# Kernel optimization log

Measured on AMD Instinct MI355X. Metric: run time of the kernel, lower is better.

Reference implementation:

```python
import jax, jax.numpy as jnp
import numpy as np

B, C, T, W, H = 4, 128, 16, 64, 64


def setup_inputs() -> dict:
    key = jax.random.key(0)
    ks = jax.random.split(key, 5)
    Cq = C // 8
    return {
        "x": jax.random.normal(ks[0], (B, C, T, W, H), jnp.float32),
        # stacked params for the 3 cells (T, W, H order, as in nn.Sequential)
        "Wq": jax.random.normal(ks[1], (3, Cq, C), jnp.float32) * 0.05,
        "bq": jnp.zeros((3, Cq), jnp.float32),
        "Wk": jax.random.normal(ks[2], (3, Cq, C), jnp.float32) * 0.05,
        "bk": jnp.zeros((3, Cq), jnp.float32),
        "Wv": jax.random.normal(ks[3], (3, C, C), jnp.float32) * 0.05,
        "bv": jnp.zeros((3, C), jnp.float32),
        # gamma is init to 0 in torch (identity); small random so the test is nontrivial
        "gamma": jax.random.normal(ks[4], (3,), jnp.float32) * 0.1,
    }


def _conv1x1(x, w, b):
    # 1x1x1 Conv3d == channel contraction
    return jnp.einsum('bcthw,oc->bothw', x, w) + b[None, :, None, None, None]


def _cell(x, wq, bq, wk, bk, wv, bv, gamma, attn_dim):
    # Faithful to torch: raw contiguous .view() == row-major reshape.
    Bb, Cc, Tt, Ww, Hh = x.shape
    q = _conv1x1(x, wq, bq).reshape(Bb, attn_dim, -1)   # (B, A, N)
    k = _conv1x1(x, wk, bk).reshape(Bb, -1, attn_dim)   # (B, N, A)  (pooling_factor=1 -> MaxPool identity)
    attn = jax.nn.softmax(jnp.matmul(q, k), axis=-1)    # (B, A, A)
    v = _conv1x1(x, wv, bv).reshape(Bb, -1, attn_dim)   # (B, M, A), M = C*T*W*H/A
    out = jnp.matmul(v, attn.swapaxes(1, 2))            # (B, M, A)
    out = out.reshape(Bb, Cc, Ww, Hh, Tt).transpose(0, 1, 4, 2, 3)  # -> (B, C, T, W, H)
    return gamma * out + x


def reference(x, Wq, bq, Wk, bk, Wv, bv, gamma):
    _, _, Tt, Ww, Hh = x.shape
    attn_dims = (Tt, Ww, Hh)  # cells with attn_id 'T', 'W', 'H'
    for i in range(3):
        x = _cell(x, Wq[i], bq[i], Wk[i], bk[i], Wv[i], bv[i], gamma[i], attn_dims[i])
    return x
```

## Files before the change

kernel.cpp:

```cpp
#include <hip/hip_runtime.h>

#define BB 4
#define CC 128
#define CQ 16
#define TDIM 16
#define SS 65536
#define CS (CC*SS)
#define NBLK 256

typedef unsigned short u16;
typedef unsigned int   u32;

typedef __bf16 bf16x8v __attribute__((ext_vector_type(8)));
typedef float  floatx4v __attribute__((ext_vector_type(4)));

__device__ __forceinline__ u16 f2bf(float f) {
    u32 u = __float_as_uint(f);
    u32 r = (u + 0x7fffu + ((u >> 16) & 1u)) >> 16;
    return (u16)r;
}
__device__ __forceinline__ void unpack8(uint4 r, float* f) {
    f[0] = __uint_as_float(r.x << 16); f[1] = __uint_as_float(r.x & 0xffff0000u);
    f[2] = __uint_as_float(r.y << 16); f[3] = __uint_as_float(r.y & 0xffff0000u);
    f[4] = __uint_as_float(r.z << 16); f[5] = __uint_as_float(r.z & 0xffff0000u);
    f[6] = __uint_as_float(r.w << 16); f[7] = __uint_as_float(r.w & 0xffff0000u);
}
__device__ __forceinline__ bf16x8v ld_bf8(const void* p) {
    union { uint4 u; bf16x8v b; } x;
    x.u = *(const uint4*)p;
    return x.b;
}

__global__ __launch_bounds__(256) void wconv_kernel(
    const float* __restrict__ Wq, const float* __restrict__ Wk, const float* __restrict__ Wv,
    const float* __restrict__ bq, const float* __restrict__ bk, const float* __restrict__ bv,
    u16* __restrict__ wbf, float* __restrict__ bias)
{
    const int idx = blockIdx.x * 256 + threadIdx.x;
    const int cell = idx / 20480;
    const int j = idx - cell * 20480;
    const int o = j >> 7, c = j & 127;
    float v;
    if (o < 16)      v = Wq[(cell * 16 + o) * 128 + c];
    else if (o < 32) v = Wk[(cell * 16 + (o - 16)) * 128 + c];
    else             v = Wv[(cell * 128 + (o - 32)) * 128 + c];
    wbf[idx] = f2bf(v);
    if (idx < 480) {
        const int cl = idx / 160, oo = idx - cl * 160;
        float b = (oo < 16) ? bq[cl * 16 + oo]
                : (oo < 32) ? bk[cl * 16 + oo - 16]
                :             bv[cl * 128 + oo - 32];
        bias[idx] = b;
    }
}

__global__ __launch_bounds__(256, 2) void qkv_mfma_kernel(
    const float* __restrict__ x,
    const u16* __restrict__ wbf, const float* __restrict__ bias,
    float* __restrict__ qf, float* __restrict__ kf, u16* __restrict__ vf)
{
    __shared__ u16 xT[128 * 128];
    const int t  = threadIdx.x;
    const int b  = blockIdx.y;
    const int s0 = blockIdx.x << 7;
    const float* xb = x + (size_t)b * CS;

    {
        const int sl = t & 127;
        const int cb = (t >> 7) << 3;
        const float* xs = xb + s0 + sl;
        const u32 rowb = (u32)sl << 8;
        const u32 swz  = (u32)(sl & 7) << 4;
#pragma unroll 2
        for (int p = 0; p < 8; p++) {
            const int c0 = p * 16 + cb;
            float f[8];
#pragma unroll
            for (int j = 0; j < 8; j++) f[j] = xs[(size_t)(c0 + j) * SS];
            uint4 pk;
            pk.x = (u32)f2bf(f[0]) | ((u32)f2bf(f[1]) << 16);
            pk.y = (u32)f2bf(f[2]) | ((u32)f2bf(f[3]) << 16);
            pk.z = (u32)f2bf(f[4]) | ((u32)f2bf(f[5]) << 16);
            pk.w = (u32)f2bf(f[6]) | ((u32)f2bf(f[7]) << 16);
            *(uint4*)((char*)xT + ((rowb + (u32)(c0 << 1)) ^ swz)) = pk;
        }
    }
    __syncthreads();

    const int lane = t & 63;
    const int wv   = t >> 6;
    const int mh   = wv >> 1;
    const int sh   = wv & 1;
    const int ln15 = lane & 15;
    const int lhi  = lane >> 4;

    floatx4v acc[5][4] = {};

    const u16* abase = wbf + ((mh * 80 + ln15) << 7) + (lhi << 3);
    const u32 swzB = (u32)(ln15 & 7) << 4;
    const int sbase = sh * 64 + ln15;

#pragma unroll
    for (int ks = 0; ks < 4; ks++) {
        bf16x8v af[5];
#pragma unroll
        for (int mi = 0; mi < 5; mi++)
            af[mi] = ld_bf8(abase + (mi << 11) + (ks << 5));
#pragma unroll
        for (int nt = 0; nt < 4; nt++) {
            const u32 off = (((u32)(sbase + nt * 16) << 8)
                           + (u32)((ks << 6) + (lhi << 4))) ^ swzB;
            bf16x8v bf = ld_bf8((const char*)xT + off);
#pragma unroll
            for (int mi = 0; mi < 5; mi++)
                acc[mi][nt] = __builtin_amdgcn_mfma_f32_16x16x32_bf16(
                                  af[mi], bf, acc[mi][nt], 0, 0, 0);
        }
    }

    float* qb = qf + (size_t)b * ((size_t)CQ * SS);
    float* kb = kf + (size_t)b * ((size_t)CQ * SS);
    u16*   vb = vf + (size_t)b * (size_t)CS;

#pragma unroll
    for (int mi = 0; mi < 5; mi++) {
        const int o0 = mh * 80 + mi * 16 + lhi * 4;
        float bia[4];
        *(float4*)bia = *(const float4*)(bias + o0);
#pragma unroll
        for (int nt = 0; nt < 4; nt++) {
            const int s = s0 + sh * 64 + nt * 16 + ln15;
            if (o0 < 16) {
#pragma unroll
                for (int r = 0; r < 4; r++)
                    qb[(size_t)(o0 + r) * SS + s] = acc[mi][nt][r] + bia[r];
            } else if (o0 < 32) {
#pragma unroll
                for (int r = 0; r < 4; r++)
                    kb[(size_t)(o0 - 16 + r) * SS + s] = acc[mi][nt][r] + bia[r];
            } else {
#pragma unroll
                for (int r = 0; r < 4; r++)
                    vb[(size_t)(o0 - 32 + r) * SS + s] = f2bf(acc[mi][nt][r] + bia[r]);
            }
        }
    }
}

template <int A>
__global__ __launch_bounds__(256) void logits_part_kernel(
    const float* __restrict__ qf, const float* __restrict__ kf,
    float* __restrict__ part)
{
    constexpr int N = (CQ * SS) / A;
    constexpr int NCHUNK = N / NBLK;
    constexpr int NLOG = (NCHUNK == 64) ? 6 : 8;
    __shared__ float qs[A][NCHUNK + 1];
    __shared__ float ks[NCHUNK][A];
    const int t  = threadIdx.x;
    const int b  = blockIdx.y;
    const int n0 = blockIdx.x << NLOG;
    const float* qb = qf + (size_t)b * ((size_t)CQ * SS);
    const float* kb = kf + (size_t)b * ((size_t)CQ * SS);

    for (int idx = t; idx < A * NCHUNK; idx += 256) {
        int a1 = idx >> NLOG, n = idx & (NCHUNK - 1);
        qs[a1][n] = qb[(size_t)a1 * N + n0 + n];
    }
    float* ksf = &ks[0][0];
    for (int idx = t; idx < NCHUNK * A; idx += 256)
        ksf[idx] = kb[(size_t)n0 * A + idx];
    __syncthreads();

    float* pb = part + ((size_t)b * NBLK + blockIdx.x) * (A * A);

    if constexpr (A == 16) {
        int a1 = t >> 4, a2 = t & 15;
        float s = 0.f;
#pragma unroll 8
        for (int n = 0; n < NCHUNK; n++) s += qs[a1][n] * ks[n][a2];
        pb[t] = s;
    } else {
        int a1  = t & 63;
        int a2b = (t >> 6) * 16;
        float acc[16];
#pragma unroll
        for (int j = 0; j < 16; j++) acc[j] = 0.f;
        for (int n = 0; n < NCHUNK; n++) {
            float q = qs[a1][n];
#pragma unroll
            for (int j = 0; j < 16; j++) acc[j] += q * ks[n][a2b + j];
        }
        float* dst = pb + t * 16;
        *(float4*)(dst)      = make_float4(acc[0],  acc[1],  acc[2],  acc[3]);
        *(float4*)(dst + 4)  = make_float4(acc[4],  acc[5],  acc[6],  acc[7]);
        *(float4*)(dst + 8)  = make_float4(acc[8],  acc[9],  acc[10], acc[11]);
        *(float4*)(dst + 12) = make_float4(acc[12], acc[13], acc[14], acc[15]);
    }
}

template <int A>
__global__ __launch_bounds__(256) void reduce_softmax_kernel(
    const float* __restrict__ part, float* __restrict__ attn)
{
    constexpr int NG = 256 / A;
    __shared__ float red[NG][A];
    const int a1 = blockIdx.x;
    const int b  = blockIdx.y;
    const int t  = threadIdx.x;
    const int a2 = t & (A - 1);
    const int g  = t >> ((A == 16) ? 4 : 6);
    const float* pb = part + (size_t)b * NBLK * (A * A);

    int off;
    if constexpr (A == 16) off = a1 * 16 + a2;
    else                   off = a1 * 16 + ((a2 >> 4) << 10) + (a2 & 15);

    float s0 = 0.f, s1 = 0.f, s2 = 0.f, s3 = 0.f;
    for (int blk = g; blk < NBLK; blk += 4 * NG) {
        s0 += pb[(size_t)(blk         ) * (A * A) + off];
        s1 += pb[(size_t)(blk +     NG) * (A * A) + off];
        s2 += pb[(size_t)(blk + 2 * NG) * (A * A) + off];
        s3 += pb[(size_t)(blk + 3 * NG) * (A * A) + off];
    }
    red[g][a2] = (s0 + s1) + (s2 + s3);
    __syncthreads();

    if (t < A) {
        float l = 0.f;
#pragma unroll
        for (int gg = 0; gg < NG; gg++) l += red[gg][t];
        float m = l;
#pragma unroll
        for (int o2 = A / 2; o2 > 0; o2 >>= 1) m = fmaxf(m, __shfl_xor(m, o2, 64));
        float e = expf(l - m);
        float s = e;
#pragma unroll
        for (int o2 = A / 2; o2 > 0; o2 >>= 1) s += __shfl_xor(s, o2, 64);
        attn[((size_t)b << 12) + a1 * A + t] = e / s;
    }
}

__global__ __launch_bounds__(256) void out16_kernel(
    const float* __restrict__ x, const u16* __restrict__ vf,
    const float* __restrict__ attn, const float* __restrict__ gptr,
    float* __restrict__ y)
{
    const int b = blockIdx.y;
    const u32 u = blockIdx.x * 256u + threadIdx.x;
    const float g = *gptr;
    const float* ab = attn + ((size_t)b << 12);
    const float* xb = x + (size_t)b * CS;
    float*       yb = y + (size_t)b * CS;
    const u16*   vr = vf + (size_t)b * CS + (size_t)u * 16;

    uint4 r0 = *(const uint4*)(vr);
    uint4 r1 = *(const uint4*)(vr + 8);
    float v0[8], v1[8];
    unpack8(r0, v0); unpack8(r1, v1);

    const size_t base = ((size_t)(u >> 12) << 16) + (u & 4095u);
#pragma unroll
    for (int tt = 0; tt < 16; tt++) {
        const float* ar = ab + tt * 16;
        float4 a0 = *(const float4*)(ar);
        float4 a1 = *(const float4*)(ar + 4);
        float4 a2 = *(const float4*)(ar + 8);
        float4 a3 = *(const float4*)(ar + 12);
        float acc = v0[0]*a0.x + v0[1]*a0.y + v0[2]*a0.z + v0[3]*a0.w
                  + v0[4]*a1.x + v0[5]*a1.y + v0[6]*a1.z + v0[7]*a1.w
                  + v1[0]*a2.x + v1[1]*a2.y + v1[2]*a2.z + v1[3]*a2.w
                  + v1[4]*a3.x + v1[5]*a3.y + v1[6]*a3.z + v1[7]*a3.w;
        const size_t i = base + ((size_t)tt << 12);
        yb[i] = g * acc + xb[i];
    }
}

__device__ __forceinline__ u32 atoff(int r, int c) {
    return (((u32)r << 8) + ((u32)c << 2)) ^ (((u32)(r >> 4) & 3u) << 4);
}

__global__ __launch_bounds__(256) void out64_kernel(
    const float* __restrict__ x, const u16* __restrict__ vf,
    const float* __restrict__ attn, const float* __restrict__ gptr,
    float* __restrict__ y)
{
    __shared__ float atf[4096];
    const int b = blockIdx.y;
    const int t = threadIdx.x;
    const float g = *gptr;
    const float* ab = attn + ((size_t)b << 12);
    {
        char* atb = (char*)atf;
        for (int idx = t; idx < 4096; idx += 256)
            *(float*)(atb + atoff(idx >> 6, idx & 63)) = ab[idx];
    }
    __syncthreads();

    const u32 u   = blockIdx.x * 256u + t;
    const int hlow = u & 3;
    const int h2   = (u >> 2) & 15;
    const int w    = (u >> 6) & 63;
    const int c    = u >> 12;
    const int n    = (c << 10) + (w << 4) + h2;

    const u16*   vr = vf + (size_t)b * CS + (size_t)n * 64;
    const float* xb = x + (size_t)b * CS;
    float*       yb = y + (size_t)b * CS;

    float acc[16];
#pragma unroll
    for (int i = 0; i < 16; i++) acc[i] = 0.f;

    const char* atb = (const char*)atf;
#pragma unroll
    for (int a2b = 0; a2b < 64; a2b += 8) {
        uint4 rv = *(const uint4*)(vr + a2b);
        float v[8];
        unpack8(rv, v);
#pragma unroll
        for (int tt = 0; tt < 16; tt++) {
            const int r = hlow * 16 + tt;
            float4 p0 = *(const float4*)(atb + atoff(r, a2b));
            float4 p1 = *(const float4*)(atb + atoff(r, a2b + 4));
            acc[tt] += v[0]*p0.x + v[1]*p0.y + v[2]*p0.z + v[3]*p0.w
                     + v[4]*p1.x + v[5]*p1.y + v[6]*p1.z + v[7]*p1.w;
        }
    }

    const size_t base = ((size_t)c << 16) + ((u32)w << 6) + (h2 << 2) + hlow;
#pragma unroll
    for (int tt = 0; tt < 16; tt++) {
        const size_t i = base + ((size_t)tt << 12);
        yb[i] = g * acc[tt] + xb[i];
    }
}

extern "C" void kernel_launch(void* const* d_in, const int* in_sizes, int n_in,
                              void* d_out, int out_size, void* d_ws, size_t ws_size,
                              hipStream_t stream)
{
    (void)in_sizes; (void)n_in; (void)out_size;
    const float* x0    = (const float*)d_in[0];
    const float* Wq    = (const float*)d_in[1];
    const float* bq    = (const float*)d_in[2];
    const float* Wk    = (const float*)d_in[3];
    const float* bk    = (const float*)d_in[4];
    const float* Wv    = (const float*)d_in[5];
    const float* bv    = (const float*)d_in[6];
    const float* gamma = (const float*)d_in[7];
    float* y = (float*)d_out;

    const size_t MiB = (size_t)1 << 20;
    const size_t need4 = 4 * (28 * MiB + 16384) + 160 * 128 * 3 * 2 + 3 * 160 * 4;
    const int nb = (ws_size >= need4) ? 4 : 1;

    char* ws = (char*)d_ws;
    float* qf    = (float*)ws;
    float* kf    = (float*)(ws + (size_t)nb * 4  * MiB);
    u16*   vf    = (u16*)  (ws + (size_t)nb * 8  * MiB);
    float* part  = (float*)(ws + (size_t)nb * 24 * MiB);
    float* attnp = (float*)(ws + (size_t)nb * 28 * MiB);
    u16*   wbf3  = (u16*)  (ws + (size_t)nb * 28 * MiB + (size_t)nb * 16384);
    float* bias3 = (float*)(ws + (size_t)nb * 28 * MiB + (size_t)nb * 16384
                               + 160 * 128 * 3 * 2);

    wconv_kernel<<<240, 256, 0, stream>>>(Wq, Wk, Wv, bq, bk, bv, wbf3, bias3);

    for (int cell = 0; cell < 3; cell++) {
        const u16*   wc = wbf3  + (size_t)cell * 160 * 128;
        const float* bc = bias3 + (size_t)cell * 160;
        for (int b0 = 0; b0 < BB; b0 += nb) {
            const float* xin = ((cell == 0) ? x0 : (const float*)y) + (size_t)b0 * CS;
            float* yb = y + (size_t)b0 * CS;

            qkv_mfma_kernel<<<dim3(512, nb), 256, 0, stream>>>(xin, wc, bc, qf, kf, vf);

            if (cell == 0) {
                logits_part_kernel<16><<<dim3(NBLK, nb), 256, 0, stream>>>(qf, kf, part);
                reduce_softmax_kernel<16><<<dim3(16, nb), 256, 0, stream>>>(part, attnp);
                out16_kernel<<<dim3(2048, nb), 256, 0, stream>>>(xin, vf, attnp, gamma + cell, yb);
            } else {
                logits_part_kernel<64><<<dim3(NBLK, nb), 256, 0, stream>>>(qf, kf, part);
                reduce_softmax_kernel<64><<<dim3(64, nb), 256, 0, stream>>>(part, attnp);
                out64_kernel<<<dim3(2048, nb), 256, 0, stream>>>(xin, vf, attnp, gamma + cell, yb);
            }
        }
    }
}
```

Before: 666.3 us.

## Use MFMA for the 64-dim attention output and widen the QKV projection blocks

The output stage of the W and H cells now does the v·attnᵀ product with bf16 MFMA instructions, replacing the scalar FMA loop that read fp32 attention from LDS. The softmax kernel writes an extra bf16 copy of the attention matrix, which is loaded straight into registers, and the output is written as float4 stores. Separately, the QKV projection kernel moves to 512 threads per block, each wave covering a smaller spatial slice with fewer accumulators. This trades cheaper compute and less register pressure for extra bf16 rounding of the attention weights, which may affect accuracy.

```diff
diff --git a/kernel.cpp b/kernel.cpp
--- a/kernel.cpp
+++ b/kernel.cpp
@@ -54,7 +54,7 @@
     }
 }
 
-__global__ __launch_bounds__(256, 2) void qkv_mfma_kernel(
+__global__ __launch_bounds__(512, 4) void qkv_mfma_kernel(
     const float* __restrict__ x,
     const u16* __restrict__ wbf, const float* __restrict__ bias,
     float* __restrict__ qf, float* __restrict__ kf, u16* __restrict__ vf)
@@ -71,9 +71,9 @@
         const float* xs = xb + s0 + sl;
         const u32 rowb = (u32)sl << 8;
         const u32 swz  = (u32)(sl & 7) << 4;
-#pragma unroll 2
-        for (int p = 0; p < 8; p++) {
-            const int c0 = p * 16 + cb;
+#pragma unroll
+        for (int p = 0; p < 4; p++) {
+            const int c0 = p * 32 + cb;
             float f[8];
 #pragma unroll
             for (int j = 0; j < 8; j++) f[j] = xs[(size_t)(c0 + j) * SS];
@@ -89,16 +89,16 @@
 
     const int lane = t & 63;
     const int wv   = t >> 6;
-    const int mh   = wv >> 1;
-    const int sh   = wv & 1;
+    const int mh   = wv >> 2;
+    const int sq   = wv & 3;
     const int ln15 = lane & 15;
     const int lhi  = lane >> 4;
 
-    floatx4v acc[5][4] = {};
+    floatx4v acc[5][2] = {};
 
     const u16* abase = wbf + ((mh * 80 + ln15) << 7) + (lhi << 3);
     const u32 swzB = (u32)(ln15 & 7) << 4;
-    const int sbase = sh * 64 + ln15;
+    const int sbase = sq * 32 + ln15;
 
 #pragma unroll
     for (int ks = 0; ks < 4; ks++) {
@@ -107,7 +107,7 @@
         for (int mi = 0; mi < 5; mi++)
             af[mi] = ld_bf8(abase + (mi << 11) + (ks << 5));
 #pragma unroll
-        for (int nt = 0; nt < 4; nt++) {
+        for (int nt = 0; nt < 2; nt++) {
             const u32 off = (((u32)(sbase + nt * 16) << 8)
                            + (u32)((ks << 6) + (lhi << 4))) ^ swzB;
             bf16x8v bf = ld_bf8((const char*)xT + off);
@@ -128,8 +128,8 @@
         float bia[4];
         *(float4*)bia = *(const float4*)(bias + o0);
 #pragma unroll
-        for (int nt = 0; nt < 4; nt++) {
-            const int s = s0 + sh * 64 + nt * 16 + ln15;
+        for (int nt = 0; nt < 2; nt++) {
+            const int s = s0 + sq * 32 + nt * 16 + ln15;
             if (o0 < 16) {
 #pragma unroll
                 for (int r = 0; r < 4; r++)
@@ -201,7 +201,7 @@
 
 template <int A>
 __global__ __launch_bounds__(256) void reduce_softmax_kernel(
-    const float* __restrict__ part, float* __restrict__ attn)
+    const float* __restrict__ part, float* __restrict__ attn, u16* __restrict__ pbf)
 {
     constexpr int NG = 256 / A;
     __shared__ float red[NG][A];
@@ -237,7 +237,10 @@
         float s = e;
 #pragma unroll
         for (int o2 = A / 2; o2 > 0; o2 >>= 1) s += __shfl_xor(s, o2, 64);
-        attn[((size_t)b << 12) + a1 * A + t] = e / s;
+        const float p = e / s;
+        attn[((size_t)b << 12) + a1 * A + t] = p;
+        if constexpr (A == 64)
+            pbf[((size_t)b << 12) + a1 * 64 + t] = f2bf(p);
     }
 }
 
@@ -276,63 +279,62 @@
     }
 }
 
-__device__ __forceinline__ u32 atoff(int r, int c) {
-    return (((u32)r << 8) + ((u32)c << 2)) ^ (((u32)(r >> 4) & 3u) << 4);
-}
-
-__global__ __launch_bounds__(256) void out64_kernel(
+__global__ __launch_bounds__(256) void out64_mfma_kernel(
     const float* __restrict__ x, const u16* __restrict__ vf,
-    const float* __restrict__ attn, const float* __restrict__ gptr,
+    const u16* __restrict__ pbf, const float* __restrict__ gptr,
     float* __restrict__ y)
 {
-    __shared__ float atf[4096];
     const int b = blockIdx.y;
     const int t = threadIdx.x;
     const float g = *gptr;
-    const float* ab = attn + ((size_t)b << 12);
-    {
-        char* atb = (char*)atf;
-        for (int idx = t; idx < 4096; idx += 256)
-            *(float*)(atb + atoff(idx >> 6, idx & 63)) = ab[idx];
-    }
-    __syncthreads();
-
-    const u32 u   = blockIdx.x * 256u + t;
-    const int hlow = u & 3;
-    const int h2   = (u >> 2) & 15;
-    const int w    = (u >> 6) & 63;
-    const int c    = u >> 12;
-    const int n    = (c << 10) + (w << 4) + h2;
-
-    const u16*   vr = vf + (size_t)b * CS + (size_t)n * 64;
+    const int lane = t & 63;
+    const int ln15 = lane & 15;
+    const int lhi  = lane >> 4;
+    const int wv   = t >> 6;
+    const int m0w  = blockIdx.x * 256 + wv * 64;
+
+    const u16*   pb = pbf + ((size_t)b << 12);
+    const u16*   vb = vf + (size_t)b * CS;
     const float* xb = x + (size_t)b * CS;
     float*       yb = y + (size_t)b * CS;
 
-    float acc[16];
-#pragma unroll
-    for (int i = 0; i < 16; i++) acc[i] = 0.f;
-
-    const char* atb = (const char*)atf;
-#pragma unroll
-    for (int a2b = 0; a2b < 64; a2b += 8) {
-        uint4 rv = *(const uint4*)(vr + a2b);
-        float v[8];
-        unpack8(rv, v);
-#pragma unroll
-        for (int tt = 0; tt < 16; tt++) {
-            const int r = hlow * 16 + tt;
-            float4 p0 = *(const float4*)(atb + atoff(r, a2b));
-            float4 p1 = *(const float4*)(atb + atoff(r, a2b + 4));
-            acc[tt] += v[0]*p0.x + v[1]*p0.y + v[2]*p0.z + v[3]*p0.w
-                     + v[4]*p1.x + v[5]*p1.y + v[6]*p1.z + v[7]*p1.w;
-        }
-    }
-
-    const size_t base = ((size_t)c << 16) + ((u32)w << 6) + (h2 << 2) + hlow;
-#pragma unroll
-    for (int tt = 0; tt < 16; tt++) {
-        const size_t i = base + ((size_t)tt << 12);
-        yb[i] = g * acc[tt] + xb[i];
+    bf16x8v af[2][4];
+#pragma unroll
+    for (int ksi = 0; ksi < 2; ksi++)
+#pragma unroll
+        for (int sub = 0; sub < 4; sub++)
+            af[ksi][sub] = ld_bf8(pb + (sub * 16 + ln15) * 64 + ksi * 32 + lhi * 8);
+
+#pragma unroll
+    for (int tile = 0; tile < 4; tile++) {
+        const int m0 = m0w + tile * 16;
+        const u16* vrow = vb + ((size_t)(m0 + ln15) << 6) + (lhi << 3);
+        bf16x8v b0 = ld_bf8(vrow);
+        bf16x8v b1 = ld_bf8(vrow + 32);
+
+        floatx4v acc[4] = {};
+#pragma unroll
+        for (int sub = 0; sub < 4; sub++) {
+            acc[sub] = __builtin_amdgcn_mfma_f32_16x16x32_bf16(af[0][sub], b0, acc[sub], 0, 0, 0);
+            acc[sub] = __builtin_amdgcn_mfma_f32_16x16x32_bf16(af[1][sub], b1, acc[sub], 0, 0, 0);
+        }
+
+        const int c   = m0 >> 10;
+        const int ow  = ((m0 >> 6) & 15) * 4 + ((m0 & 63) >> 4);
+        const size_t base = ((size_t)c << 16) + ((size_t)ow << 6) + (size_t)(ln15 << 2);
+        const float* xbase = xb + base;
+        float*       ybase = yb + base;
+#pragma unroll
+        for (int r = 0; r < 4; r++) {
+            const int ot = lhi * 4 + r;
+            float4 xv = *(const float4*)(xbase + ((size_t)ot << 12));
+            float4 o;
+            o.x = g * acc[0][r] + xv.x;
+            o.y = g * acc[1][r] + xv.y;
+            o.z = g * acc[2][r] + xv.z;
+            o.w = g * acc[3][r] + xv.w;
+            *(float4*)(ybase + ((size_t)ot << 12)) = o;
+        }
     }
 }
 
@@ -352,7 +354,7 @@
     float* y = (float*)d_out;
 
     const size_t MiB = (size_t)1 << 20;
-    const size_t need4 = 4 * (28 * MiB + 16384) + 160 * 128 * 3 * 2 + 3 * 160 * 4;
+    const size_t need4 = 4 * (28 * MiB + 16384 + 8192) + 160 * 128 * 3 * 2 + 3 * 160 * 4;
     const int nb = (ws_size >= need4) ? 4 : 1;
 
     char* ws = (char*)d_ws;
@@ -361,8 +363,9 @@
     u16*   vf    = (u16*)  (ws + (size_t)nb * 8  * MiB);
     float* part  = (float*)(ws + (size_t)nb * 24 * MiB);
     float* attnp = (float*)(ws + (size_t)nb * 28 * MiB);
-    u16*   wbf3  = (u16*)  (ws + (size_t)nb * 28 * MiB + (size_t)nb * 16384);
-    float* bias3 = (float*)(ws + (size_t)nb * 28 * MiB + (size_t)nb * 16384
+    u16*   pbf   = (u16*)  (ws + (size_t)nb * 28 * MiB + (size_t)nb * 16384);
+    u16*   wbf3  = (u16*)  (ws + (size_t)nb * 28 * MiB + (size_t)nb * (16384 + 8192));
+    float* bias3 = (float*)(ws + (size_t)nb * 28 * MiB + (size_t)nb * (16384 + 8192)
                                + 160 * 128 * 3 * 2);
 
     wconv_kernel<<<240, 256, 0, stream>>>(Wq, Wk, Wv, bq, bk, bv, wbf3, bias3);
@@ -374,16 +377,16 @@
             const float* xin = ((cell == 0) ? x0 : (const float*)y) + (size_t)b0 * CS;
             float* yb = y + (size_t)b0 * CS;
 
-            qkv_mfma_kernel<<<dim3(512, nb), 256, 0, stream>>>(xin, wc, bc, qf, kf, vf);
+            qkv_mfma_kernel<<<dim3(512, nb), 512, 0, stream>>>(xin, wc, bc, qf, kf, vf);
 
             if (cell == 0) {
                 logits_part_kernel<16><<<dim3(NBLK, nb), 256, 0, stream>>>(qf, kf, part);
-                reduce_softmax_kernel<16><<<dim3(16, nb), 256, 0, stream>>>(part, attnp);
+                reduce_softmax_kernel<16><<<dim3(16, nb), 256, 0, stream>>>(part, attnp, pbf);
                 out16_kernel<<<dim3(2048, nb), 256, 0, stream>>>(xin, vf, attnp, gamma + cell, yb);
             } else {
                 logits_part_kernel<64><<<dim3(NBLK, nb), 256, 0, stream>>>(qf, kf, part);
-                reduce_softmax_kernel<64><<<dim3(64, nb), 256, 0, stream>>>(part, attnp);
-                out64_kernel<<<dim3(2048, nb), 256, 0, stream>>>(xin, vf, attnp, gamma + cell, yb);
+                reduce_softmax_kernel<64><<<dim3(64, nb), 256, 0, stream>>>(part, attnp, pbf);
+                out64_mfma_kernel<<<dim3(512, nb), 256, 0, stream>>>(xin, vf, pbf, gamma + cell, yb);
             }
         }
     }
```

New measurement: 630.1 us. 5.4% less time.
